# Performance work log

Hardware: AMD Instinct MI355X
Metric: run time of the kernel (lower is better)

## Reference

```python
import jax, jax.numpy as jnp
import numpy as np

N = 100000
E = 1600000
D_IN = 128
D_OUT = 128
EPS = 1e-5


def setup_inputs() -> dict:
    key = jax.random.key(0)
    ks = jax.random.split(key, 8)
    x = jax.random.normal(ks[0], (N, D_IN), dtype=jnp.float32)
    edge_index = jax.random.randint(ks[1], (2, E), 0, N, dtype=jnp.int64)
    s1 = 1.0 / np.sqrt(D_IN)
    s2 = 1.0 / np.sqrt(D_OUT)
    W1 = jax.random.uniform(ks[2], (D_IN, D_OUT), jnp.float32, -s1, s1)
    b1 = jax.random.uniform(ks[3], (D_OUT,), jnp.float32, -s1, s1)
    W2 = jax.random.uniform(ks[4], (D_OUT, D_OUT), jnp.float32, -s2, s2)
    b2 = jax.random.uniform(ks[5], (D_OUT,), jnp.float32, -s2, s2)
    gamma = jnp.ones((D_OUT,), jnp.float32)
    beta = jnp.zeros((D_OUT,), jnp.float32)
    return {"x": x, "edge_index": edge_index, "W1": W1, "b1": b1,
            "W2": W2, "b2": b2, "gamma": gamma, "beta": beta}


def reference(x, edge_index, W1, b1, W2, b2, gamma, beta):
    row, col = edge_index[0], edge_index[1]
    # scatter-add neighbor aggregation: agg[row] += x[col]
    agg = jax.ops.segment_sum(x[col], row, num_segments=N)
    h = x + agg  # residual (self) + aggregated neighbors
    # MLP: Linear -> ReLU -> Linear -> BatchNorm1d (training-mode batch stats)
    h = jax.nn.relu(h @ W1 + b1)
    h = h @ W2 + b2
    mean = jnp.mean(h, axis=0)
    var = jnp.mean(jnp.square(h - mean), axis=0)  # biased var, as torch BN uses
    out = gamma * (h - mean) * jax.lax.rsqrt(var + EPS) + beta
    return out
```

## Files before the change

kernel.cpp:

```cpp
#include <hip/hip_runtime.h>

#define N_NODES 100000
#define N_EDGES 1600000
#define DIM     128
#define EPS_BN  1e-5f
#define NB      512
#define NPB     196
#define NBLK    256
#define EPB     6250
#define CAP     4096
#define M_TILE  64
#define M_PAD   100032
#define GBLK    1563
#define LPITCH  136

typedef __attribute__((ext_vector_type(8))) short short8;
typedef __attribute__((ext_vector_type(4))) float floatx4;

__device__ __forceinline__ unsigned short f2bf(float f) {
    unsigned u = __float_as_uint(f);
    return (unsigned short)((u + 0x7FFF + ((u >> 16) & 1)) >> 16);
}
__device__ __forceinline__ float bf2f(unsigned short b) {
    return __uint_as_float((unsigned)b << 16);
}

__device__ __forceinline__ int detect64(const void* eidx) {
    int v = ((const int*)eidx)[2 * (threadIdx.x & 63) + 1];
    unsigned long long b = __ballot(v != 0);
    return (b == 0ULL) ? 1 : 0;
}
__device__ __forceinline__ int load_row(const void* eidx, int is64, int e) {
    if (is64) return (int)((const long long*)eidx)[e];
    return ((const int*)eidx)[e];
}
__device__ __forceinline__ int load_col(const void* eidx, int is64, int e) {
    if (is64) return (int)((const long long*)eidx)[N_EDGES + e];
    return ((const int*)eidx)[N_EDGES + e];
}

__global__ void convert_w(const float* __restrict__ W1,
                          const float* __restrict__ W2,
                          unsigned short* __restrict__ W1t,
                          unsigned short* __restrict__ W2t,
                          int* __restrict__ bcur, float* __restrict__ gstats) {
    if (blockIdx.x == 2) {
        int t = threadIdx.x;
        bcur[t] = 0;
        bcur[256 + t] = 0;
        if (t < 2 * DIM) gstats[t] = 0.f;
        return;
    }
    const float* W = blockIdx.x ? W2 : W1;
    unsigned short* Wt = blockIdx.x ? W2t : W1t;
    for (int i = threadIdx.x; i < DIM * DIM; i += 256) {
        int k = i >> 7, n = i & 127;
        Wt[n * DIM + k] = f2bf(W[i]);
    }
}

__global__ __launch_bounds__(1024) void bin_scatter_x(
    const void* eidx, int* bcur, unsigned* __restrict__ slots,
    const float* __restrict__ x, unsigned short* __restrict__ xb) {
    __shared__ int lh[NB];
    __shared__ int lbase[NB];
    __shared__ int loff[NB];
    __shared__ unsigned stage[EPB];
    __shared__ int gaddr[EPB];
    int t = threadIdx.x;
    int is64 = detect64(eidx);
    if (t < NB) lh[t] = 0;
    __syncthreads();
    int base = blockIdx.x * EPB;
    for (int i = t; i < EPB; i += 1024) {
        int r = load_row(eidx, is64, base + i);
        atomicAdd(&lh[r / NPB], 1);
    }
    __syncthreads();
    if (t < NB) loff[t] = lh[t];
    __syncthreads();
    for (int off = 1; off < NB; off <<= 1) {
        int a = (t >= off && t < NB) ? loff[t - off] : 0;
        __syncthreads();
        if (t < NB) loff[t] += a;
        __syncthreads();
    }
    if (t < NB) {
        int c = lh[t];
        lbase[t] = c ? atomicAdd(&bcur[t], c) : 0;
        loff[t] -= c;
        lh[t] = 0;
    }
    __syncthreads();
    for (int i = t; i < EPB; i += 1024) {
        int r = load_row(eidx, is64, base + i);
        int c = load_col(eidx, is64, base + i);
        int b = r / NPB;
        int pos = atomicAdd(&lh[b], 1);
        int idx = loff[b] + pos;
        int ga = lbase[b] + pos;
        if (ga >= CAP) ga = CAP - 1;
        stage[idx] = ((unsigned)(r - b * NPB) << 24) | (unsigned)c;
        gaddr[idx] = b * CAP + ga;
    }
    __syncthreads();
    for (int i = t; i < EPB; i += 1024)
        slots[gaddr[i]] = stage[i];
    for (int i = blockIdx.x * 1024 + t; i < N_NODES * DIM / 4; i += NBLK * 1024) {
        float4 v = ((const float4*)x)[i];
        ushort4 o;
        o.x = f2bf(v.x); o.y = f2bf(v.y); o.z = f2bf(v.z); o.w = f2bf(v.w);
        ((ushort4*)xb)[i] = o;
    }
}

__global__ __launch_bounds__(1024, 8) void csr_agg(
    const unsigned short* __restrict__ xb,
    const unsigned* __restrict__ slots,
    const int* __restrict__ bcnt,
    unsigned short* __restrict__ Hbf) {
    __shared__ int hist[256];
    __shared__ int incl[256];
    __shared__ int cur[256];
    __shared__ int colbuf[CAP];
    int t = threadIdx.x;
    int b = blockIdx.x;
    int cnt = bcnt[b];
    if (cnt > CAP) cnt = CAP;
    if (cnt < 0) cnt = 0;
    int node0 = b * NPB;
    int nn = N_NODES - node0;
    if (nn > NPB) nn = NPB;
    if (nn < 0) nn = 0;
    const unsigned* pairs = slots + (size_t)b * CAP;
    if (t < 256) hist[t] = 0;
    __syncthreads();
    for (int i = t; i < cnt; i += 1024)
        atomicAdd(&hist[(int)(pairs[i] >> 24)], 1);
    __syncthreads();
    int v = (t < 256) ? hist[t] : 0;
    if (t < 256) incl[t] = v;
    __syncthreads();
    for (int off = 1; off < 256; off <<= 1) {
        int a = (t >= off && t < 256) ? incl[t - off] : 0;
        __syncthreads();
        if (t < 256) incl[t] += a;
        __syncthreads();
    }
    if (t < 256) cur[t] = incl[t] - v;
    __syncthreads();
    for (int i = t; i < cnt; i += 1024) {
        unsigned pr = pairs[i];
        int pos = atomicAdd(&cur[pr >> 24], 1);
        if (pos < CAP) colbuf[pos] = (int)(pr & 0xFFFFFFu);
    }
    __syncthreads();

    const unsigned* xbw = (const unsigned*)xb;
    int lane = t & 63, wv = t >> 6;
    for (int nl = wv; nl < nn; nl += 16) {
        int node = node0 + nl;
        unsigned selfw = xbw[(size_t)node * 64 + lane];
        float2 acc;
        acc.x = __uint_as_float(selfw << 16);
        acc.y = __uint_as_float(selfw & 0xffff0000u);
        int e = incl[nl];
        int s = nl ? incl[nl - 1] : 0;
        s = __builtin_amdgcn_readfirstlane(s);
        e = __builtin_amdgcn_readfirstlane(e);
        int d = e - s;
        if (d <= 16) {
            unsigned pw[16];
#pragma unroll
            for (int u = 0; u < 16; ++u) {
                int idx = s + u;
                int ci = (idx < e) ? idx : s;
                pw[u] = xbw[(size_t)colbuf[ci] * 64 + lane];
            }
#pragma unroll
            for (int u = 0; u < 16; ++u) {
                unsigned w = (u < d) ? pw[u] : 0u;
                acc.x += __uint_as_float(w << 16);
                acc.y += __uint_as_float(w & 0xffff0000u);
            }
        } else {
            int j = s;
            for (; j + 16 <= e; j += 16) {
                unsigned pw[16];
#pragma unroll
                for (int u = 0; u < 16; ++u)
                    pw[u] = xbw[(size_t)colbuf[j + u] * 64 + lane];
#pragma unroll
                for (int u = 0; u < 16; ++u) {
                    acc.x += __uint_as_float(pw[u] << 16);
                    acc.y += __uint_as_float(pw[u] & 0xffff0000u);
                }
            }
            if (j < e) {
                unsigned pw[16];
                int dd = e - j;
#pragma unroll
                for (int u = 0; u < 16; ++u) {
                    int idx = j + u;
                    int ci = (idx < e) ? idx : s;
                    pw[u] = xbw[(size_t)colbuf[ci] * 64 + lane];
                }
#pragma unroll
                for (int u = 0; u < 16; ++u) {
                    unsigned w = (u < dd) ? pw[u] : 0u;
                    acc.x += __uint_as_float(w << 16);
                    acc.y += __uint_as_float(w & 0xffff0000u);
                }
            }
        }
        unsigned pack = (unsigned)f2bf(acc.x) | ((unsigned)f2bf(acc.y) << 16);
        ((unsigned*)Hbf)[(size_t)node * 64 + lane] = pack;
    }
}

__global__ __launch_bounds__(256) void mlp_fused(
    const unsigned short* __restrict__ A,
    const unsigned short* __restrict__ B1t,
    const unsigned short* __restrict__ B2t,
    const float* __restrict__ bias1, const float* __restrict__ bias2,
    unsigned short* __restrict__ outb,
    float* __restrict__ gpart) {
    __shared__ unsigned short As[M_TILE * LPITCH];
    __shared__ unsigned short Bs[DIM * LPITCH];
    int t = threadIdx.x;
    int row0 = blockIdx.x * M_TILE;
    int lane = t & 63, wv = t >> 6;
    int m = lane & 15, g = lane >> 4;

#pragma unroll
    for (int i = 0; i < 4; ++i) {
        int ch = t + 256 * i;
        int r = ch >> 4, cc = ch & 15;
        *(uint4*)(&As[r * LPITCH + cc * 8]) =
            *(const uint4*)(&A[(size_t)(row0 + r) * DIM + cc * 8]);
    }
#pragma unroll
    for (int i = 0; i < 8; ++i) {
        int ch = t + 256 * i;
        int n = ch >> 4, cc = ch & 15;
        *(uint4*)(&Bs[n * LPITCH + cc * 8]) =
            *(const uint4*)(&B1t[n * DIM + cc * 8]);
    }
    __syncthreads();

    floatx4 acc1[8] = {};
#pragma unroll
    for (int kc = 0; kc < 4; ++kc) {
        short8 a = *(const short8*)(&As[(wv * 16 + m) * LPITCH + kc * 32 + g * 8]);
#pragma unroll
        for (int tt = 0; tt < 8; ++tt) {
            short8 b = *(const short8*)(&Bs[(tt * 16 + m) * LPITCH + kc * 32 + g * 8]);
            acc1[tt] = __builtin_amdgcn_mfma_f32_16x16x32_bf16(a, b, acc1[tt], 0, 0, 0);
        }
    }
    __syncthreads();

    uint4 wbuf[8];
#pragma unroll
    for (int i = 0; i < 8; ++i) {
        int ch = t + 256 * i;
        int n = ch >> 4, cc = ch & 15;
        wbuf[i] = *(const uint4*)(&B2t[n * DIM + cc * 8]);
    }
#pragma unroll
    for (int tt = 0; tt < 8; ++tt) {
        int col = tt * 16 + m;
        float bv = bias1[col];
#pragma unroll
        for (int j = 0; j < 4; ++j) {
            int rl = wv * 16 + g * 4 + j;
            As[rl * LPITCH + col] = f2bf(fmaxf(acc1[tt][j] + bv, 0.f));
        }
    }
#pragma unroll
    for (int i = 0; i < 8; ++i) {
        int ch = t + 256 * i;
        int n = ch >> 4, cc = ch & 15;
        *(uint4*)(&Bs[n * LPITCH + cc * 8]) = wbuf[i];
    }
    __syncthreads();

    floatx4 acc2[8] = {};
#pragma unroll
    for (int kc = 0; kc < 4; ++kc) {
        short8 a = *(const short8*)(&As[(wv * 16 + m) * LPITCH + kc * 32 + g * 8]);
#pragma unroll
        for (int tt = 0; tt < 8; ++tt) {
            short8 b = *(const short8*)(&Bs[(tt * 16 + m) * LPITCH + kc * 32 + g * 8]);
            acc2[tt] = __builtin_amdgcn_mfma_f32_16x16x32_bf16(a, b, acc2[tt], 0, 0, 0);
        }
    }

    float* csum = (float*)As;
    float* csq = csum + DIM;
    __syncthreads();
    if (t < DIM) { csum[t] = 0.f; csq[t] = 0.f; }
    __syncthreads();
#pragma unroll
    for (int tt = 0; tt < 8; ++tt) {
        int col = tt * 16 + m;
        float bv = bias2[col];
        float s = 0.f, q = 0.f;
#pragma unroll
        for (int j = 0; j < 4; ++j) {
            int row = row0 + wv * 16 + g * 4 + j;
            float v = acc2[tt][j] + bv;
            outb[(size_t)row * DIM + col] = f2bf(v);
            if (row < N_NODES) { s += v; q += v * v; }
        }
        atomicAdd(&csum[col], s);
        atomicAdd(&csq[col], q);
    }
    __syncthreads();
    gpart[(size_t)blockIdx.x * 256 + t] = (t < DIM) ? csum[t] : csq[t - DIM];
}

__global__ __launch_bounds__(256) void reduce_stats(
    const float* __restrict__ gpart, float* __restrict__ gstats) {
    int t = threadIdx.x;
    int chunk = (GBLK + 31) / 32;
    int r0 = blockIdx.x * chunk;
    int r1 = r0 + chunk < GBLK ? r0 + chunk : GBLK;
    float s = 0.f;
    for (int r = r0; r < r1; ++r) s += gpart[(size_t)r * 256 + t];
    atomicAdd(&gstats[t], s);
}

__global__ __launch_bounds__(256) void bn_apply(
    const unsigned short* __restrict__ H2, const float* __restrict__ gstats,
    const float* __restrict__ gamma, const float* __restrict__ beta,
    float* __restrict__ out) {
    __shared__ float sc_s[DIM], sh_s[DIM];
    int t = threadIdx.x;
    if (t < DIM) {
        float mean = gstats[t] * (1.0f / N_NODES);
        float m2 = gstats[DIM + t] * (1.0f / N_NODES);
        float var = m2 - mean * mean;
        float inv = rsqrtf(var + EPS_BN);
        float sc = gamma[t] * inv;
        sc_s[t] = sc;
        sh_s[t] = beta[t] - mean * sc;
    }
    __syncthreads();
    int i = blockIdx.x * 256 + t;
    int j4 = (i & 31) * 4;
    ushort4 hv = ((const ushort4*)H2)[i];
    float4 o;
    o.x = bf2f(hv.x) * sc_s[j4 + 0] + sh_s[j4 + 0];
    o.y = bf2f(hv.y) * sc_s[j4 + 1] + sh_s[j4 + 1];
    o.z = bf2f(hv.z) * sc_s[j4 + 2] + sh_s[j4 + 2];
    o.w = bf2f(hv.w) * sc_s[j4 + 3] + sh_s[j4 + 3];
    ((float4*)out)[i] = o;
}

extern "C" void kernel_launch(void* const* d_in, const int* in_sizes, int n_in,
                              void* d_out, int out_size, void* d_ws,
                              size_t ws_size, hipStream_t stream) {
    (void)in_sizes; (void)n_in; (void)out_size; (void)ws_size;
    const float* x     = (const float*)d_in[0];
    const void*  eidx  = d_in[1];
    const float* W1    = (const float*)d_in[2];
    const float* b1    = (const float*)d_in[3];
    const float* W2    = (const float*)d_in[4];
    const float* b2    = (const float*)d_in[5];
    const float* gamma = (const float*)d_in[6];
    const float* beta  = (const float*)d_in[7];
    float* out = (float*)d_out;

    char* p = (char*)d_ws;
    auto alloc = [&](size_t bytes) {
        char* r = p;
        p += (bytes + 255) & ~(size_t)255;
        return r;
    };
    unsigned short* Hbf  = (unsigned short*)alloc((size_t)M_PAD * DIM * 2);
    unsigned short* h2bf = (unsigned short*)alloc((size_t)M_PAD * DIM * 2);
    unsigned* slots = (unsigned*)h2bf;
    unsigned short* xb = (unsigned short*)alloc((size_t)N_NODES * DIM * 2);
    float* gpart  = (float*)alloc((size_t)GBLK * 256 * 4);
    int*   bcur   = (int*)alloc(NB * 4);
    unsigned short* W1t = (unsigned short*)alloc(DIM * DIM * 2);
    unsigned short* W2t = (unsigned short*)alloc(DIM * DIM * 2);
    float* gstats = (float*)alloc(2 * DIM * 4);

    convert_w<<<3, 256, 0, stream>>>(W1, W2, W1t, W2t, bcur, gstats);
    bin_scatter_x<<<NBLK, 1024, 0, stream>>>(eidx, bcur, slots, x, xb);
    csr_agg<<<NB, 1024, 0, stream>>>(xb, slots, bcur, Hbf);

    mlp_fused<<<GBLK, 256, 0, stream>>>(Hbf, W1t, W2t, b1, b2, h2bf, gpart);
    reduce_stats<<<32, 256, 0, stream>>>(gpart, gstats);
    bn_apply<<<(N_NODES * DIM / 4) / 256, 256, 0, stream>>>(h2bf, gstats,
                                                            gamma, beta, out);
}
```

Measured before the change: 285.0 us.

## Fuse neighbor aggregation with MLP per node bin and fold weight conversion into scatter

Result: faster. 264.1 us (-7.4%).

```diff
diff --git a/kernel.cpp b/kernel.cpp
--- a/kernel.cpp
+++ b/kernel.cpp
@@ -4,14 +4,13 @@
 #define N_EDGES 1600000
 #define DIM     128
 #define EPS_BN  1e-5f
-#define NB      512
-#define NPB     196
+#define NB      1024
+#define NPB     98
 #define NBLK    256
 #define EPB     6250
-#define CAP     4096
-#define M_TILE  64
-#define M_PAD   100032
-#define GBLK    1563
+#define CAP     2048
+#define PADR    112
+#define NT      7
 #define LPITCH  136
 
 typedef __attribute__((ext_vector_type(8))) short short8;
@@ -39,29 +38,11 @@
     return ((const int*)eidx)[N_EDGES + e];
 }
 
-__global__ void convert_w(const float* __restrict__ W1,
-                          const float* __restrict__ W2,
-                          unsigned short* __restrict__ W1t,
-                          unsigned short* __restrict__ W2t,
-                          int* __restrict__ bcur, float* __restrict__ gstats) {
-    if (blockIdx.x == 2) {
-        int t = threadIdx.x;
-        bcur[t] = 0;
-        bcur[256 + t] = 0;
-        if (t < 2 * DIM) gstats[t] = 0.f;
-        return;
-    }
-    const float* W = blockIdx.x ? W2 : W1;
-    unsigned short* Wt = blockIdx.x ? W2t : W1t;
-    for (int i = threadIdx.x; i < DIM * DIM; i += 256) {
-        int k = i >> 7, n = i & 127;
-        Wt[n * DIM + k] = f2bf(W[i]);
-    }
-}
-
-__global__ __launch_bounds__(1024) void bin_scatter_x(
+__global__ __launch_bounds__(1024) void bin_scatter_xw(
     const void* eidx, int* bcur, unsigned* __restrict__ slots,
-    const float* __restrict__ x, unsigned short* __restrict__ xb) {
+    const float* __restrict__ x, unsigned short* __restrict__ xb,
+    const float* __restrict__ W1, const float* __restrict__ W2,
+    unsigned short* __restrict__ W1t, unsigned short* __restrict__ W2t) {
     __shared__ int lh[NB];
     __shared__ int lbase[NB];
     __shared__ int loff[NB];
@@ -69,7 +50,7 @@
     __shared__ int gaddr[EPB];
     int t = threadIdx.x;
     int is64 = detect64(eidx);
-    if (t < NB) lh[t] = 0;
+    lh[t] = 0;
     __syncthreads();
     int base = blockIdx.x * EPB;
     for (int i = t; i < EPB; i += 1024) {
@@ -77,15 +58,15 @@
         atomicAdd(&lh[r / NPB], 1);
     }
     __syncthreads();
-    if (t < NB) loff[t] = lh[t];
+    loff[t] = lh[t];
     __syncthreads();
     for (int off = 1; off < NB; off <<= 1) {
-        int a = (t >= off && t < NB) ? loff[t - off] : 0;
+        int a = (t >= off) ? loff[t - off] : 0;
         __syncthreads();
-        if (t < NB) loff[t] += a;
+        loff[t] += a;
         __syncthreads();
     }
-    if (t < NB) {
+    {
         int c = lh[t];
         lbase[t] = c ? atomicAdd(&bcur[t], c) : 0;
         loff[t] -= c;
@@ -106,6 +87,14 @@
     __syncthreads();
     for (int i = t; i < EPB; i += 1024)
         slots[gaddr[i]] = stage[i];
+    if (blockIdx.x < 2) {
+        const float* W = blockIdx.x ? W2 : W1;
+        unsigned short* Wt = blockIdx.x ? W2t : W1t;
+        for (int i = t; i < DIM * DIM; i += 1024) {
+            int k = i >> 7, n = i & 127;
+            Wt[n * DIM + k] = f2bf(W[i]);
+        }
+    }
     for (int i = blockIdx.x * 1024 + t; i < N_NODES * DIM / 4; i += NBLK * 1024) {
         float4 v = ((const float4*)x)[i];
         ushort4 o;
@@ -114,17 +103,25 @@
     }
 }
 
-__global__ __launch_bounds__(1024, 8) void csr_agg(
+__global__ __launch_bounds__(1024, 8) void csr_agg_mlp(
     const unsigned short* __restrict__ xb,
     const unsigned* __restrict__ slots,
     const int* __restrict__ bcnt,
-    unsigned short* __restrict__ Hbf) {
-    __shared__ int hist[256];
-    __shared__ int incl[256];
-    __shared__ int cur[256];
+    const unsigned short* __restrict__ B1t,
+    const unsigned short* __restrict__ B2t,
+    const float* __restrict__ bias1, const float* __restrict__ bias2,
+    unsigned short* __restrict__ h2,
+    float* __restrict__ gpart) {
+    __shared__ int hist[128];
+    __shared__ int incl[128];
+    __shared__ int cur[128];
     __shared__ int colbuf[CAP];
+    __shared__ unsigned short As[PADR * LPITCH];
+    __shared__ unsigned short Bs[DIM * LPITCH];
     int t = threadIdx.x;
     int b = blockIdx.x;
+    int lane = t & 63, wv = t >> 6;
+    int m = lane & 15, g = lane >> 4;
     int cnt = bcnt[b];
     if (cnt > CAP) cnt = CAP;
     if (cnt < 0) cnt = 0;
@@ -133,21 +130,29 @@
     if (nn > NPB) nn = NPB;
     if (nn < 0) nn = 0;
     const unsigned* pairs = slots + (size_t)b * CAP;
-    if (t < 256) hist[t] = 0;
+
+#pragma unroll
+    for (int i = 0; i < 2; ++i) {
+        int ch = t + 1024 * i;
+        int n = ch >> 4, cc = ch & 15;
+        *(uint4*)(&Bs[n * LPITCH + cc * 8]) =
+            *(const uint4*)(&B1t[n * DIM + cc * 8]);
+    }
+    if (t < 128) hist[t] = 0;
     __syncthreads();
     for (int i = t; i < cnt; i += 1024)
         atomicAdd(&hist[(int)(pairs[i] >> 24)], 1);
     __syncthreads();
-    int v = (t < 256) ? hist[t] : 0;
-    if (t < 256) incl[t] = v;
-    __syncthreads();
-    for (int off = 1; off < 256; off <<= 1) {
-        int a = (t >= off && t < 256) ? incl[t - off] : 0;
+    int v = (t < 128) ? hist[t] : 0;
+    if (t < 128) incl[t] = v;
+    __syncthreads();
+    for (int off = 1; off < 128; off <<= 1) {
+        int a = (t >= off && t < 128) ? incl[t - off] : 0;
         __syncthreads();
-        if (t < 256) incl[t] += a;
+        if (t < 128) incl[t] += a;
         __syncthreads();
     }
-    if (t < 256) cur[t] = incl[t] - v;
+    if (t < 128) cur[t] = incl[t] - v;
     __syncthreads();
     for (int i = t; i < cnt; i += 1024) {
         unsigned pr = pairs[i];
@@ -157,177 +162,153 @@
     __syncthreads();
 
     const unsigned* xbw = (const unsigned*)xb;
-    int lane = t & 63, wv = t >> 6;
-    for (int nl = wv; nl < nn; nl += 16) {
-        int node = node0 + nl;
-        unsigned selfw = xbw[(size_t)node * 64 + lane];
-        float2 acc;
-        acc.x = __uint_as_float(selfw << 16);
-        acc.y = __uint_as_float(selfw & 0xffff0000u);
-        int e = incl[nl];
-        int s = nl ? incl[nl - 1] : 0;
-        s = __builtin_amdgcn_readfirstlane(s);
-        e = __builtin_amdgcn_readfirstlane(e);
-        int d = e - s;
-        if (d <= 16) {
-            unsigned pw[16];
-#pragma unroll
-            for (int u = 0; u < 16; ++u) {
-                int idx = s + u;
-                int ci = (idx < e) ? idx : s;
-                pw[u] = xbw[(size_t)colbuf[ci] * 64 + lane];
-            }
-#pragma unroll
-            for (int u = 0; u < 16; ++u) {
-                unsigned w = (u < d) ? pw[u] : 0u;
-                acc.x += __uint_as_float(w << 16);
-                acc.y += __uint_as_float(w & 0xffff0000u);
-            }
-        } else {
-            int j = s;
-            for (; j + 16 <= e; j += 16) {
+    for (int nl = wv; nl < PADR; nl += 16) {
+        unsigned pack = 0u;
+        if (nl < nn) {
+            int node = node0 + nl;
+            unsigned selfw = xbw[(size_t)node * 64 + lane];
+            float ax = __uint_as_float(selfw << 16);
+            float ay = __uint_as_float(selfw & 0xffff0000u);
+            int e = incl[nl];
+            int s = nl ? incl[nl - 1] : 0;
+            s = __builtin_amdgcn_readfirstlane(s);
+            e = __builtin_amdgcn_readfirstlane(e);
+            int d = e - s;
+            if (d <= 16) {
                 unsigned pw[16];
 #pragma unroll
-                for (int u = 0; u < 16; ++u)
-                    pw[u] = xbw[(size_t)colbuf[j + u] * 64 + lane];
-#pragma unroll
                 for (int u = 0; u < 16; ++u) {
-                    acc.x += __uint_as_float(pw[u] << 16);
-                    acc.y += __uint_as_float(pw[u] & 0xffff0000u);
-                }
-            }
-            if (j < e) {
-                unsigned pw[16];
-                int dd = e - j;
-#pragma unroll
-                for (int u = 0; u < 16; ++u) {
-                    int idx = j + u;
+                    int idx = s + u;
                     int ci = (idx < e) ? idx : s;
                     pw[u] = xbw[(size_t)colbuf[ci] * 64 + lane];
                 }
 #pragma unroll
                 for (int u = 0; u < 16; ++u) {
-                    unsigned w = (u < dd) ? pw[u] : 0u;
-                    acc.x += __uint_as_float(w << 16);
-                    acc.y += __uint_as_float(w & 0xffff0000u);
-                }
-            }
-        }
-        unsigned pack = (unsigned)f2bf(acc.x) | ((unsigned)f2bf(acc.y) << 16);
-        ((unsigned*)Hbf)[(size_t)node * 64 + lane] = pack;
-    }
-}
-
-__global__ __launch_bounds__(256) void mlp_fused(
-    const unsigned short* __restrict__ A,
-    const unsigned short* __restrict__ B1t,
-    const unsigned short* __restrict__ B2t,
-    const float* __restrict__ bias1, const float* __restrict__ bias2,
-    unsigned short* __restrict__ outb,
-    float* __restrict__ gpart) {
-    __shared__ unsigned short As[M_TILE * LPITCH];
-    __shared__ unsigned short Bs[DIM * LPITCH];
-    int t = threadIdx.x;
-    int row0 = blockIdx.x * M_TILE;
-    int lane = t & 63, wv = t >> 6;
-    int m = lane & 15, g = lane >> 4;
-
-#pragma unroll
-    for (int i = 0; i < 4; ++i) {
-        int ch = t + 256 * i;
-        int r = ch >> 4, cc = ch & 15;
-        *(uint4*)(&As[r * LPITCH + cc * 8]) =
-            *(const uint4*)(&A[(size_t)(row0 + r) * DIM + cc * 8]);
-    }
-#pragma unroll
-    for (int i = 0; i < 8; ++i) {
-        int ch = t + 256 * i;
+                    unsigned w = (u < d) ? pw[u] : 0u;
+                    ax += __uint_as_float(w << 16);
+                    ay += __uint_as_float(w & 0xffff0000u);
+                }
+            } else {
+                int j = s;
+                for (; j + 16 <= e; j += 16) {
+                    unsigned pw[16];
+#pragma unroll
+                    for (int u = 0; u < 16; ++u)
+                        pw[u] = xbw[(size_t)colbuf[j + u] * 64 + lane];
+#pragma unroll
+                    for (int u = 0; u < 16; ++u) {
+                        ax += __uint_as_float(pw[u] << 16);
+                        ay += __uint_as_float(pw[u] & 0xffff0000u);
+                    }
+                }
+                if (j < e) {
+                    unsigned pw[16];
+                    int dd = e - j;
+#pragma unroll
+                    for (int u = 0; u < 16; ++u) {
+                        int idx = j + u;
+                        int ci = (idx < e) ? idx : s;
+                        pw[u] = xbw[(size_t)colbuf[ci] * 64 + lane];
+                    }
+#pragma unroll
+                    for (int u = 0; u < 16; ++u) {
+                        unsigned w = (u < dd) ? pw[u] : 0u;
+                        ax += __uint_as_float(w << 16);
+                        ay += __uint_as_float(w & 0xffff0000u);
+                    }
+                }
+            }
+            pack = (unsigned)f2bf(ax) | ((unsigned)f2bf(ay) << 16);
+        }
+        *(unsigned*)(&As[nl * LPITCH + lane * 2]) = pack;
+    }
+    __syncthreads();
+
+    floatx4 acc1[8];
+    if (wv < NT) {
+#pragma unroll
+        for (int tt = 0; tt < 8; ++tt) acc1[tt] = (floatx4){0.f, 0.f, 0.f, 0.f};
+#pragma unroll
+        for (int kc = 0; kc < 4; ++kc) {
+            short8 a = *(const short8*)(&As[(wv * 16 + m) * LPITCH + kc * 32 + g * 8]);
+#pragma unroll
+            for (int tt = 0; tt < 8; ++tt) {
+                short8 bb = *(const short8*)(&Bs[(tt * 16 + m) * LPITCH + kc * 32 + g * 8]);
+                acc1[tt] = __builtin_amdgcn_mfma_f32_16x16x32_bf16(a, bb, acc1[tt], 0, 0, 0);
+            }
+        }
+    }
+    __syncthreads();
+
+    if (wv < NT) {
+#pragma unroll
+        for (int tt = 0; tt < 8; ++tt) {
+            int col = tt * 16 + m;
+            float bv = bias1[col];
+#pragma unroll
+            for (int j = 0; j < 4; ++j) {
+                int rl = wv * 16 + g * 4 + j;
+                As[rl * LPITCH + col] = f2bf(fmaxf(acc1[tt][j] + bv, 0.f));
+            }
+        }
+    }
+#pragma unroll
+    for (int i = 0; i < 2; ++i) {
+        int ch = t + 1024 * i;
         int n = ch >> 4, cc = ch & 15;
         *(uint4*)(&Bs[n * LPITCH + cc * 8]) =
-            *(const uint4*)(&B1t[n * DIM + cc * 8]);
-    }
-    __syncthreads();
-
-    floatx4 acc1[8] = {};
-#pragma unroll
-    for (int kc = 0; kc < 4; ++kc) {
-        short8 a = *(const short8*)(&As[(wv * 16 + m) * LPITCH + kc * 32 + g * 8]);
-#pragma unroll
-        for (int tt = 0; tt < 8; ++tt) {
-            short8 b = *(const short8*)(&Bs[(tt * 16 + m) * LPITCH + kc * 32 + g * 8]);
-            acc1[tt] = __builtin_amdgcn_mfma_f32_16x16x32_bf16(a, b, acc1[tt], 0, 0, 0);
-        }
-    }
-    __syncthreads();
-
-    uint4 wbuf[8];
-#pragma unroll
-    for (int i = 0; i < 8; ++i) {
-        int ch = t + 256 * i;
-        int n = ch >> 4, cc = ch & 15;
-        wbuf[i] = *(const uint4*)(&B2t[n * DIM + cc * 8]);
-    }
-#pragma unroll
-    for (int tt = 0; tt < 8; ++tt) {
-        int col = tt * 16 + m;
-        float bv = bias1[col];
-#pragma unroll
-        for (int j = 0; j < 4; ++j) {
-            int rl = wv * 16 + g * 4 + j;
-            As[rl * LPITCH + col] = f2bf(fmaxf(acc1[tt][j] + bv, 0.f));
-        }
-    }
-#pragma unroll
-    for (int i = 0; i < 8; ++i) {
-        int ch = t + 256 * i;
-        int n = ch >> 4, cc = ch & 15;
-        *(uint4*)(&Bs[n * LPITCH + cc * 8]) = wbuf[i];
-    }
-    __syncthreads();
-
-    floatx4 acc2[8] = {};
-#pragma unroll
-    for (int kc = 0; kc < 4; ++kc) {
-        short8 a = *(const short8*)(&As[(wv * 16 + m) * LPITCH + kc * 32 + g * 8]);
-#pragma unroll
-        for (int tt = 0; tt < 8; ++tt) {
-            short8 b = *(const short8*)(&Bs[(tt * 16 + m) * LPITCH + kc * 32 + g * 8]);
-            acc2[tt] = __builtin_amdgcn_mfma_f32_16x16x32_bf16(a, b, acc2[tt], 0, 0, 0);
-        }
-    }
-
-    float* csum = (float*)As;
-    float* csq = csum + DIM;
-    __syncthreads();
-    if (t < DIM) { csum[t] = 0.f; csq[t] = 0.f; }
-    __syncthreads();
-#pragma unroll
-    for (int tt = 0; tt < 8; ++tt) {
-        int col = tt * 16 + m;
-        float bv = bias2[col];
-        float s = 0.f, q = 0.f;
-#pragma unroll
-        for (int j = 0; j < 4; ++j) {
-            int row = row0 + wv * 16 + g * 4 + j;
-            float v = acc2[tt][j] + bv;
-            outb[(size_t)row * DIM + col] = f2bf(v);
-            if (row < N_NODES) { s += v; q += v * v; }
-        }
-        atomicAdd(&csum[col], s);
-        atomicAdd(&csq[col], q);
-    }
-    __syncthreads();
-    gpart[(size_t)blockIdx.x * 256 + t] = (t < DIM) ? csum[t] : csq[t - DIM];
+            *(const uint4*)(&B2t[n * DIM + cc * 8]);
+    }
+    float* csum = (float*)colbuf;
+    if (t < 256) csum[t] = 0.f;
+    __syncthreads();
+
+    if (wv < NT) {
+#pragma unroll
+        for (int hg = 0; hg < 2; ++hg) {
+            floatx4 acc2[4];
+#pragma unroll
+            for (int q = 0; q < 4; ++q) acc2[q] = (floatx4){0.f, 0.f, 0.f, 0.f};
+#pragma unroll
+            for (int kc = 0; kc < 4; ++kc) {
+                short8 a = *(const short8*)(&As[(wv * 16 + m) * LPITCH + kc * 32 + g * 8]);
+#pragma unroll
+                for (int q = 0; q < 4; ++q) {
+                    int tile = hg * 4 + q;
+                    short8 bb = *(const short8*)(&Bs[(tile * 16 + m) * LPITCH + kc * 32 + g * 8]);
+                    acc2[q] = __builtin_amdgcn_mfma_f32_16x16x32_bf16(a, bb, acc2[q], 0, 0, 0);
+                }
+            }
+#pragma unroll
+            for (int q = 0; q < 4; ++q) {
+                int col = (hg * 4 + q) * 16 + m;
+                float bv = bias2[col];
+                float s = 0.f, qq = 0.f;
+#pragma unroll
+                for (int j = 0; j < 4; ++j) {
+                    int rl = wv * 16 + g * 4 + j;
+                    if (rl < nn) {
+                        float vv = acc2[q][j] + bv;
+                        h2[(size_t)(node0 + rl) * DIM + col] = f2bf(vv);
+                        s += vv; qq += vv * vv;
+                    }
+                }
+                atomicAdd(&csum[col], s);
+                atomicAdd(&csum[DIM + col], qq);
+            }
+        }
+    }
+    __syncthreads();
+    if (t < 256) gpart[(size_t)b * 256 + t] = csum[t];
 }
 
 __global__ __launch_bounds__(256) void reduce_stats(
     const float* __restrict__ gpart, float* __restrict__ gstats) {
     int t = threadIdx.x;
-    int chunk = (GBLK + 31) / 32;
+    int chunk = NB / 32;
     int r0 = blockIdx.x * chunk;
-    int r1 = r0 + chunk < GBLK ? r0 + chunk : GBLK;
     float s = 0.f;
-    for (int r = r0; r < r1; ++r) s += gpart[(size_t)r * 256 + t];
+    for (int r = r0; r < r0 + chunk; ++r) s += gpart[(size_t)r * 256 + t];
     atomicAdd(&gstats[t], s);
 }
 
@@ -378,21 +359,20 @@
         p += (bytes + 255) & ~(size_t)255;
         return r;
     };
-    unsigned short* Hbf  = (unsigned short*)alloc((size_t)M_PAD * DIM * 2);
-    unsigned short* h2bf = (unsigned short*)alloc((size_t)M_PAD * DIM * 2);
-    unsigned* slots = (unsigned*)h2bf;
+    unsigned short* h2bf = (unsigned short*)alloc((size_t)N_NODES * DIM * 2);
+    unsigned* slots = (unsigned*)alloc((size_t)NB * CAP * 4);
     unsigned short* xb = (unsigned short*)alloc((size_t)N_NODES * DIM * 2);
-    float* gpart  = (float*)alloc((size_t)GBLK * 256 * 4);
-    int*   bcur   = (int*)alloc(NB * 4);
+    float* gpart  = (float*)alloc((size_t)NB * 256 * 4);
+    int*   bcur   = (int*)alloc(NB * 4 + 2 * DIM * 4);
+    float* gstats = (float*)(bcur + NB);
     unsigned short* W1t = (unsigned short*)alloc(DIM * DIM * 2);
     unsigned short* W2t = (unsigned short*)alloc(DIM * DIM * 2);
-    float* gstats = (float*)alloc(2 * DIM * 4);
-
-    convert_w<<<3, 256, 0, stream>>>(W1, W2, W1t, W2t, bcur, gstats);
-    bin_scatter_x<<<NBLK, 1024, 0, stream>>>(eidx, bcur, slots, x, xb);
-    csr_agg<<<NB, 1024, 0, stream>>>(xb, slots, bcur, Hbf);
-
-    mlp_fused<<<GBLK, 256, 0, stream>>>(Hbf, W1t, W2t, b1, b2, h2bf, gpart);
+
+    hipMemsetAsync(bcur, 0, NB * 4 + 2 * DIM * 4, stream);
+    bin_scatter_xw<<<NBLK, 1024, 0, stream>>>(eidx, bcur, slots, x, xb,
+                                              W1, W2, W1t, W2t);
+    csr_agg_mlp<<<NB, 1024, 0, stream>>>(xb, slots, bcur, W1t, W2t, b1, b2,
+                                         h2bf, gpart);
     reduce_stats<<<32, 256, 0, stream>>>(gpart, gstats);
     bn_apply<<<(N_NODES * DIM / 4) / 256, 256, 0, stream>>>(h2bf, gstats,
                                                             gamma, beta, out);
```
